# Kernel tuning notes

Hardware: AMD Instinct MI355X
Metric: run time of the kernel (lower is better)

## Reference

```python
import jax, jax.numpy as jnp
import numpy as np

EMB = 1024
HEADS = 16
HEAD_DIM = EMB // HEADS
EPS = 1e-5


def gelu_tanh(x):
    c = jnp.sqrt(jnp.asarray(2.0 / jnp.pi, x.dtype))
    return 0.5 * x * (1.0 + jnp.tanh(c * (x + 0.044715 * x ** 3)))


def layernorm(x, scale, shift):
    mean = jnp.mean(x, axis=-1, keepdims=True)
    var = jnp.mean((x - mean) ** 2, axis=-1, keepdims=True)
    return scale * (x - mean) / jnp.sqrt(var + EPS) + shift


def setup_inputs() -> dict:
    key = jax.random.key(0)
    ks = jax.random.split(key, 12)
    s = 0.02
    return {
        "x": jax.random.normal(ks[0], (2, 2048, EMB), dtype=jnp.float32),
        "Wq": jax.random.normal(ks[1], (EMB, EMB), dtype=jnp.float32) * s,
        "Wk": jax.random.normal(ks[2], (EMB, EMB), dtype=jnp.float32) * s,
        "Wv": jax.random.normal(ks[3], (EMB, EMB), dtype=jnp.float32) * s,
        "Wo": jax.random.normal(ks[4], (EMB, EMB), dtype=jnp.float32) * s,
        "bo": jnp.zeros((EMB,), dtype=jnp.float32),
        "W1": jax.random.normal(ks[5], (EMB, 4 * EMB), dtype=jnp.float32) * s,
        "b1": jnp.zeros((4 * EMB,), dtype=jnp.float32),
        "W2": jax.random.normal(ks[6], (4 * EMB, EMB), dtype=jnp.float32) * s,
        "b2": jnp.zeros((EMB,), dtype=jnp.float32),
        "ln1_scale": jnp.ones((EMB,), dtype=jnp.float32),
        "ln1_shift": jnp.zeros((EMB,), dtype=jnp.float32),
        "ln2_scale": jnp.ones((EMB,), dtype=jnp.float32),
        "ln2_shift": jnp.zeros((EMB,), dtype=jnp.float32),
    }


def reference(x, Wq, Wk, Wv, Wo, bo, W1, b1, W2, b2,
              ln1_scale, ln1_shift, ln2_scale, ln2_shift):
    b, n, d = x.shape
    # --- attention sublayer (pre-LN) ---
    h = layernorm(x, ln1_scale, ln1_shift)
    q = (h @ Wq).reshape(b, n, HEADS, HEAD_DIM).transpose(0, 2, 1, 3)  # [b,h,n,hd]
    k = (h @ Wk).reshape(b, n, HEADS, HEAD_DIM).transpose(0, 2, 1, 3)
    v = (h @ Wv).reshape(b, n, HEADS, HEAD_DIM).transpose(0, 2, 1, 3)
    scores = jnp.einsum('bhqd,bhkd->bhqk', q, k)  # [b,h,n,n]
    causal = jnp.tril(jnp.ones((n, n), dtype=bool))  # True = keep
    scores = jnp.where(causal, scores, -jnp.inf)
    weights = jax.nn.softmax(scores / np.sqrt(HEAD_DIM), axis=-1)
    ctx = jnp.einsum('bhqk,bhkd->bqhd', weights, v).reshape(b, n, d)
    attn_out = ctx @ Wo + bo
    x = x + attn_out
    # --- FFN sublayer (pre-LN) ---
    h = layernorm(x, ln2_scale, ln2_shift)
    h = gelu_tanh(h @ W1 + b1) @ W2 + b2
    return x + h
```

## Files before the change

### kernel.cpp

```cpp
#include <hip/hip_runtime.h>
#include <hip/hip_bf16.h>


using bf16 = __hip_bfloat16;
using bf16x8 = __attribute__((ext_vector_type(8))) short;
using f32x4 = __attribute__((ext_vector_type(4))) float;

#define MFMA16(a, b, c) __builtin_amdgcn_mfma_f32_16x16x32_bf16((a), (b), (c), 0, 0, 0)

enum { EPI_BF16 = 0, EPI_BIAS_RES_F32 = 1, EPI_GELU_BF16 = 2 };

__device__ __forceinline__ float cvt_f(float x) { return x; }
__device__ __forceinline__ float cvt_f(bf16 x) { return __bfloat162float(x); }

__device__ __forceinline__ float gelu_f(float x) {
  float z = 0.7978845608028654f * (x + 0.044715f * x * x * x);
  z = fminf(fmaxf(z, -15.f), 15.f);
  float e = __expf(2.f * z);
  return 0.5f * x * (1.f + (e - 1.f) / (e + 1.f));
}

__device__ __forceinline__ void stage16(const bf16* g, bf16* lds_base, int lane) {
#if defined(__has_builtin) && __has_builtin(__builtin_amdgcn_global_load_lds)
  __builtin_amdgcn_global_load_lds(
      (__attribute__((address_space(1))) void*)(void*)g,
      (__attribute__((address_space(3))) void*)lds_base, 16, 0, 0);
#else
  *(int4*)(lds_base + lane * 8) = *(const int4*)g;
#endif
}

template <typename T>
__global__ __launch_bounds__(256) void transpose_bf16_k(
    const T* __restrict__ src, bf16* __restrict__ dst, int sld, int dld) {
  __shared__ float tile[32][33];
  const int tx = threadIdx.x & 31, ty = threadIdx.x >> 5;
  const size_t r0 = (size_t)blockIdx.y * 32, c0 = (size_t)blockIdx.x * 32;
#pragma unroll
  for (int i = 0; i < 32; i += 8)
    tile[ty + i][tx] = cvt_f(src[(r0 + ty + i) * sld + c0 + tx]);
  __syncthreads();
#pragma unroll
  for (int i = 0; i < 32; i += 8)
    dst[(c0 + ty + i) * dld + r0 + tx] = __float2bfloat16(tile[tx][ty + i]);
}

__global__ __launch_bounds__(256) void ln_fwd_k(
    const float* __restrict__ x, const float* __restrict__ gam,
    const float* __restrict__ bet, bf16* __restrict__ out) {
  const int row = blockIdx.x;
  const float4 v = ((const float4*)(x + (size_t)row * 1024))[threadIdx.x];
  float s = v.x + v.y + v.z + v.w;
  float sq = v.x * v.x + v.y * v.y + v.z * v.z + v.w * v.w;
#pragma unroll
  for (int off = 32; off; off >>= 1) {
    s += __shfl_down(s, off);
    sq += __shfl_down(sq, off);
  }
  __shared__ float rs[4], rq[4];
  const int w = threadIdx.x >> 6, lane = threadIdx.x & 63;
  if (lane == 0) { rs[w] = s; rq[w] = sq; }
  __syncthreads();
  s = rs[0] + rs[1] + rs[2] + rs[3];
  sq = rq[0] + rq[1] + rq[2] + rq[3];
  const float mean = s * (1.f / 1024.f);
  const float var = sq * (1.f / 1024.f) - mean * mean;
  const float rstd = rsqrtf(var + 1e-5f);
  const float4 g4 = ((const float4*)gam)[threadIdx.x];
  const float4 b4 = ((const float4*)bet)[threadIdx.x];
  short4 pk;
  bf16* hp = (bf16*)&pk;
  hp[0] = __float2bfloat16((v.x - mean) * rstd * g4.x + b4.x);
  hp[1] = __float2bfloat16((v.y - mean) * rstd * g4.y + b4.y);
  hp[2] = __float2bfloat16((v.z - mean) * rstd * g4.z + b4.z);
  hp[3] = __float2bfloat16((v.w - mean) * rstd * g4.w + b4.w);
  ((short4*)(out + (size_t)row * 1024))[threadIdx.x] = pk;
}

template <int EPI, int BN>
__global__ __launch_bounds__(256) void gemm_bt_k(
    const bf16* __restrict__ A, const bf16* __restrict__ BT,
    void* __restrict__ Cout, const float* __restrict__ bias,
    const float* __restrict__ res, int M, int N, int K) {
  constexpr int WC = BN / 64;
  constexpr int MI = 2 * WC;
  __shared__ bf16 As[128 * 64];
  __shared__ bf16 Bs[BN * 64];
  const int tid = threadIdx.x;
  const int w = tid >> 6, lane = tid & 63;
  const int wc = w % WC, wr = w / WC;
  const int lr = lane & 15, lk = lane >> 4;
  const size_t rowTile = (size_t)blockIdx.y * 128;
  const size_t colTile = (size_t)blockIdx.x * BN;

  const bf16* Ag = A + rowTile * K;
  const bf16* Bg = BT + colTile * K;
  const int srow = lane >> 3;
  const int scol = (lane & 7) * 8;

  const f32x4 z4 = {0.f, 0.f, 0.f, 0.f};
  f32x4 acc[MI][4];
#pragma unroll
  for (int i = 0; i < MI; ++i)
#pragma unroll
    for (int j = 0; j < 4; ++j) acc[i][j] = z4;

  for (int kb = 0; kb < K; kb += 64) {
#pragma unroll
    for (int i = 0; i < 4; ++i) {
      const int r = w * 32 + i * 8;
      stage16(Ag + (size_t)(r + srow) * K + kb + scol, &As[r * 64], lane);
    }
#pragma unroll
    for (int i = 0; i < BN / 32; ++i) {
      const int r = w * (BN / 4) + i * 8;
      stage16(Bg + (size_t)(r + srow) * K + kb + scol, &Bs[r * 64], lane);
    }
    __syncthreads();
#pragma unroll
    for (int kk = 0; kk < 2; ++kk) {
      bf16x8 af[MI], bg[4];
#pragma unroll
      for (int mi = 0; mi < MI; ++mi)
        af[mi] = *(const bf16x8*)&As[(wr * (32 * WC) + mi * 16 + lr) * 64 + kk * 32 + lk * 8];
#pragma unroll
      for (int ni = 0; ni < 4; ++ni)
        bg[ni] = *(const bf16x8*)&Bs[(wc * 64 + ni * 16 + lr) * 64 + kk * 32 + lk * 8];
#pragma unroll
      for (int mi = 0; mi < MI; ++mi)
#pragma unroll
        for (int ni = 0; ni < 4; ++ni)
          acc[mi][ni] = MFMA16(af[mi], bg[ni], acc[mi][ni]);
    }
    __syncthreads();
  }

  const size_t baseRow = rowTile + wr * (32 * WC);
  const size_t baseCol = colTile + wc * 64;
#pragma unroll
  for (int mi = 0; mi < MI; ++mi)
#pragma unroll
    for (int ni = 0; ni < 4; ++ni) {
      const size_t col = baseCol + ni * 16 + lr;
#pragma unroll
      for (int r = 0; r < 4; ++r) {
        const size_t row = baseRow + mi * 16 + lk * 4 + r;
        const size_t idx = row * (size_t)N + col;
        const float v = acc[mi][ni][r];
        if constexpr (EPI == EPI_BF16) {
          ((bf16*)Cout)[idx] = __float2bfloat16(v);
        } else if constexpr (EPI == EPI_BIAS_RES_F32) {
          ((float*)Cout)[idx] = v + bias[col] + res[idx];
        } else {
          ((bf16*)Cout)[idx] = __float2bfloat16(gelu_f(v + bias[col]));
        }
      }
    }
}

__global__ __launch_bounds__(256) void attn_fwd_k(
    const bf16* __restrict__ QKV, const bf16* __restrict__ VT,
    bf16* __restrict__ ctx) {
  const int qp = blockIdx.x, head = blockIdx.y, batch = blockIdx.z;
  const int tid = threadIdx.x;
  const int w = tid >> 6, lane = tid & 63;
  const int lr = lane & 15, lk = lane >> 4;
  const int qbA = qp, qbB = 31 - qp;
  const int qrowA = qbA * 64 + w * 16;
  const int qrowB = qbB * 64 + w * 16;

  __shared__ bf16 Ks[64 * 64];
  __shared__ bf16 Vs[64 * 64];
  __shared__ bf16 Ps[4][16 * 64];

  const bf16* qpa = QKV + (size_t)(batch * 2048 + qrowA + lr) * 3072 + head * 64 + lk * 8;
  const bf16* qpb = QKV + (size_t)(batch * 2048 + qrowB + lr) * 3072 + head * 64 + lk * 8;
  const bf16x8 aqA0 = *(const bf16x8*)qpa, aqA1 = *(const bf16x8*)(qpa + 32);
  const bf16x8 aqB0 = *(const bf16x8*)qpb, aqB1 = *(const bf16x8*)(qpb + 32);

  const f32x4 z4 = {0.f, 0.f, 0.f, 0.f};
  float mA[4], lA[4], mB[4], lB[4];
  f32x4 coA[4], coB[4];
#pragma unroll
  for (int r = 0; r < 4; ++r) { mA[r] = mB[r] = -1e30f; lA[r] = lB[r] = 0.f; }
#pragma unroll
  for (int nd = 0; nd < 4; ++nd) { coA[nd] = z4; coB[nd] = z4; }

  const bf16* kbase = QKV + (size_t)(batch * 2048) * 3072 + 1024 + head * 64;
  const bf16* vbase = VT + (size_t)(head * 64) * 4096 + batch * 2048;
  const int srow = tid >> 3;
  const int scol = (tid & 7) * 8;
  const int swoff = ((tid & 7) ^ (srow & 7)) * 8;
  const int eQ = (lk ^ (lr & 7)) << 3;

  auto attn_step = [&](int qrow_w, bool diag, int kb64, float* m0, float* l0,
                       f32x4* co, bf16x8 aq0, bf16x8 aq1) {
    f32x4 sv[4];
#pragma unroll
    for (int ni = 0; ni < 4; ++ni) {
      const bf16x8 bk0 = *(const bf16x8*)&Ks[(ni * 16 + lr) * 64 + eQ];
      const bf16x8 bk1 = *(const bf16x8*)&Ks[(ni * 16 + lr) * 64 + (eQ ^ 32)];
      f32x4 z = z4;
      z = MFMA16(aq0, bk0, z);
      z = MFMA16(aq1, bk1, z);
      sv[ni] = z;
    }
#pragma unroll
    for (int ni = 0; ni < 4; ++ni)
#pragma unroll
      for (int r = 0; r < 4; ++r) {
        float v = sv[ni][r] * 0.125f;
        if (diag && (kb64 + ni * 16 + lr > qrow_w + lk * 4 + r)) v = -1e30f;
        sv[ni][r] = v;
      }
    float fac[4];
#pragma unroll
    for (int r = 0; r < 4; ++r) {
      float mx = fmaxf(fmaxf(sv[0][r], sv[1][r]), fmaxf(sv[2][r], sv[3][r]));
      mx = fmaxf(mx, __shfl_xor(mx, 1));
      mx = fmaxf(mx, __shfl_xor(mx, 2));
      mx = fmaxf(mx, __shfl_xor(mx, 4));
      mx = fmaxf(mx, __shfl_xor(mx, 8));
      const float mn = fmaxf(m0[r], mx);
      fac[r] = __expf(m0[r] - mn);
      m0[r] = mn;
    }
#pragma unroll
    for (int ni = 0; ni < 4; ++ni)
#pragma unroll
      for (int r = 0; r < 4; ++r) sv[ni][r] = __expf(sv[ni][r] - m0[r]);
#pragma unroll
    for (int r = 0; r < 4; ++r) {
      float ps = sv[0][r] + sv[1][r] + sv[2][r] + sv[3][r];
      ps += __shfl_xor(ps, 1);
      ps += __shfl_xor(ps, 2);
      ps += __shfl_xor(ps, 4);
      ps += __shfl_xor(ps, 8);
      l0[r] = l0[r] * fac[r] + ps;
    }
#pragma unroll
    for (int ni = 0; ni < 4; ++ni)
#pragma unroll
      for (int r = 0; r < 4; ++r) {
        const int prow = lk * 4 + r;
        const int pcol = (((ni * 2 + (lr >> 3)) ^ (prow & 7)) << 3) + (lr & 7);
        Ps[w][prow * 64 + pcol] = __float2bfloat16(sv[ni][r]);
      }
#pragma unroll
    for (int nd = 0; nd < 4; ++nd)
#pragma unroll
      for (int r = 0; r < 4; ++r) co[nd][r] *= fac[r];
#pragma unroll
    for (int kk = 0; kk < 2; ++kk) {
      const int ep = kk ? (eQ ^ 32) : eQ;
      const bf16x8 ap = *(const bf16x8*)&Ps[w][lr * 64 + ep];
#pragma unroll
      for (int nd = 0; nd < 4; ++nd) {
        const bf16x8 bv = *(const bf16x8*)&Vs[(nd * 16 + lr) * 64 + ep];
        co[nd] = MFMA16(ap, bv, co[nd]);
      }
    }
  };

  for (int kb = 0; kb <= qbB; ++kb) {
    const int kb64 = kb * 64;
    *(int4*)&Ks[srow * 64 + swoff]        = *(const int4*)&kbase[(size_t)(kb64 + srow) * 3072 + scol];
    *(int4*)&Ks[(srow + 32) * 64 + swoff] = *(const int4*)&kbase[(size_t)(kb64 + srow + 32) * 3072 + scol];
    *(int4*)&Vs[srow * 64 + swoff]        = *(const int4*)&vbase[(size_t)srow * 4096 + kb64 + scol];
    *(int4*)&Vs[(srow + 32) * 64 + swoff] = *(const int4*)&vbase[(size_t)(srow + 32) * 4096 + kb64 + scol];
    __syncthreads();

    attn_step(qrowB, kb == qbB, kb64, mB, lB, coB, aqB0, aqB1);
    if (kb <= qbA)
      attn_step(qrowA, kb == qbA, kb64, mA, lA, coA, aqA0, aqA1);
    __syncthreads();
  }

#pragma unroll
  for (int nd = 0; nd < 4; ++nd)
#pragma unroll
    for (int r = 0; r < 4; ++r) {
      const size_t rowA = (size_t)(batch * 2048 + qrowA + lk * 4 + r);
      ctx[rowA * 1024 + head * 64 + nd * 16 + lr] = __float2bfloat16(coA[nd][r] / lA[r]);
      const size_t rowB = (size_t)(batch * 2048 + qrowB + lk * 4 + r);
      ctx[rowB * 1024 + head * 64 + nd * 16 + lr] = __float2bfloat16(coB[nd][r] / lB[r]);
    }
}

extern "C" void kernel_launch(void* const* d_in, const int* in_sizes, int n_in,
                              void* d_out, int out_size, void* d_ws, size_t ws_size,
                              hipStream_t stream) {
  const float* x    = (const float*)d_in[0];
  const float* Wq   = (const float*)d_in[1];
  const float* Wk   = (const float*)d_in[2];
  const float* Wv   = (const float*)d_in[3];
  const float* Wo   = (const float*)d_in[4];
  const float* bo   = (const float*)d_in[5];
  const float* W1   = (const float*)d_in[6];
  const float* b1   = (const float*)d_in[7];
  const float* W2   = (const float*)d_in[8];
  const float* b2   = (const float*)d_in[9];
  const float* ln1s = (const float*)d_in[10];
  const float* ln1b = (const float*)d_in[11];
  const float* ln2s = (const float*)d_in[12];
  const float* ln2b = (const float*)d_in[13];
  float* out = (float*)d_out;

  char* ws = (char*)d_ws;
  const size_t MB = 1ull << 20;
  bf16* WqkvT = (bf16*)(ws + 0);
  bf16* WoT   = (bf16*)(ws + 6 * MB);
  bf16* W1T   = (bf16*)(ws + 8 * MB);
  bf16* W2T   = (bf16*)(ws + 16 * MB);
  bf16* h1    = (bf16*)(ws + 24 * MB);
  bf16* QKV   = (bf16*)(ws + 32 * MB);
  bf16* VT    = (bf16*)(ws + 56 * MB);
  bf16* f1    = (bf16*)(ws + 32 * MB);
  bf16* ctx   = (bf16*)(ws + 64 * MB);

  const dim3 T(256);

  transpose_bf16_k<float><<<dim3(32, 32), T, 0, stream>>>(Wq, WqkvT, 1024, 1024);
  transpose_bf16_k<float><<<dim3(32, 32), T, 0, stream>>>(Wk, WqkvT + 1024 * 1024, 1024, 1024);
  transpose_bf16_k<float><<<dim3(32, 32), T, 0, stream>>>(Wv, WqkvT + 2048 * 1024, 1024, 1024);
  transpose_bf16_k<float><<<dim3(32, 32), T, 0, stream>>>(Wo, WoT, 1024, 1024);
  transpose_bf16_k<float><<<dim3(128, 32), T, 0, stream>>>(W1, W1T, 4096, 1024);
  transpose_bf16_k<float><<<dim3(32, 128), T, 0, stream>>>(W2, W2T, 1024, 4096);

  ln_fwd_k<<<4096, T, 0, stream>>>(x, ln1s, ln1b, h1);

  gemm_bt_k<EPI_BF16, 128><<<dim3(24, 32), T, 0, stream>>>(
      h1, WqkvT, QKV, nullptr, nullptr, 4096, 3072, 1024);

  transpose_bf16_k<bf16><<<dim3(32, 128), T, 0, stream>>>(QKV + 2048, VT, 3072, 4096);

  attn_fwd_k<<<dim3(16, 16, 2), T, 0, stream>>>(QKV, VT, ctx);

  gemm_bt_k<EPI_BIAS_RES_F32, 64><<<dim3(16, 32), T, 0, stream>>>(
      ctx, WoT, out, bo, x, 4096, 1024, 1024);

  ln_fwd_k<<<4096, T, 0, stream>>>(out, ln2s, ln2b, h1);

  gemm_bt_k<EPI_GELU_BF16, 128><<<dim3(32, 32), T, 0, stream>>>(
      h1, W1T, f1, b1, nullptr, 4096, 4096, 1024);

  gemm_bt_k<EPI_BIAS_RES_F32, 64><<<dim3(16, 32), T, 0, stream>>>(
      f1, W2T, out, b2, out, 4096, 1024, 4096);
}
```

Before: 424.3 us.

## Split paired-query attention blocks into one query block per workgroup, use exp2

```diff
diff --git a/kernel.cpp b/kernel.cpp
--- a/kernel.cpp
+++ b/kernel.cpp
@@ -12,6 +12,14 @@
 
 __device__ __forceinline__ float cvt_f(float x) { return x; }
 __device__ __forceinline__ float cvt_f(bf16 x) { return __bfloat162float(x); }
+
+__device__ __forceinline__ float fast_exp2(float x) {
+#if defined(__has_builtin) && __has_builtin(__builtin_amdgcn_exp2f)
+  return __builtin_amdgcn_exp2f(x);
+#else
+  return exp2f(x);
+#endif
+}
 
 __device__ __forceinline__ float gelu_f(float x) {
   float z = 0.7978845608028654f * (x + 0.044715f * x * x * x);
@@ -161,30 +169,28 @@
 __global__ __launch_bounds__(256) void attn_fwd_k(
     const bf16* __restrict__ QKV, const bf16* __restrict__ VT,
     bf16* __restrict__ ctx) {
-  const int qp = blockIdx.x, head = blockIdx.y, batch = blockIdx.z;
+  const int qb = 31 - blockIdx.x;
+  const int head = blockIdx.y, batch = blockIdx.z;
   const int tid = threadIdx.x;
   const int w = tid >> 6, lane = tid & 63;
   const int lr = lane & 15, lk = lane >> 4;
-  const int qbA = qp, qbB = 31 - qp;
-  const int qrowA = qbA * 64 + w * 16;
-  const int qrowB = qbB * 64 + w * 16;
+  const int qrow_w = qb * 64 + w * 16;
 
   __shared__ bf16 Ks[64 * 64];
   __shared__ bf16 Vs[64 * 64];
   __shared__ bf16 Ps[4][16 * 64];
 
-  const bf16* qpa = QKV + (size_t)(batch * 2048 + qrowA + lr) * 3072 + head * 64 + lk * 8;
-  const bf16* qpb = QKV + (size_t)(batch * 2048 + qrowB + lr) * 3072 + head * 64 + lk * 8;
-  const bf16x8 aqA0 = *(const bf16x8*)qpa, aqA1 = *(const bf16x8*)(qpa + 32);
-  const bf16x8 aqB0 = *(const bf16x8*)qpb, aqB1 = *(const bf16x8*)(qpb + 32);
+  const bf16* qp = QKV + (size_t)(batch * 2048 + qrow_w + lr) * 3072 + head * 64 + lk * 8;
+  const bf16x8 aq0 = *(const bf16x8*)qp;
+  const bf16x8 aq1 = *(const bf16x8*)(qp + 32);
 
   const f32x4 z4 = {0.f, 0.f, 0.f, 0.f};
-  float mA[4], lA[4], mB[4], lB[4];
-  f32x4 coA[4], coB[4];
-#pragma unroll
-  for (int r = 0; r < 4; ++r) { mA[r] = mB[r] = -1e30f; lA[r] = lB[r] = 0.f; }
-#pragma unroll
-  for (int nd = 0; nd < 4; ++nd) { coA[nd] = z4; coB[nd] = z4; }
+  float m0[4], l0[4];
+  f32x4 co[4];
+#pragma unroll
+  for (int r = 0; r < 4; ++r) { m0[r] = -1e30f; l0[r] = 0.f; }
+#pragma unroll
+  for (int nd = 0; nd < 4; ++nd) co[nd] = z4;
 
   const bf16* kbase = QKV + (size_t)(batch * 2048) * 3072 + 1024 + head * 64;
   const bf16* vbase = VT + (size_t)(head * 64) * 4096 + batch * 2048;
@@ -193,8 +199,16 @@
   const int swoff = ((tid & 7) ^ (srow & 7)) * 8;
   const int eQ = (lk ^ (lr & 7)) << 3;
 
-  auto attn_step = [&](int qrow_w, bool diag, int kb64, float* m0, float* l0,
-                       f32x4* co, bf16x8 aq0, bf16x8 aq1) {
+  const float SCALE = 0.125f * 1.44269504f;
+
+  for (int kb = 0; kb <= qb; ++kb) {
+    const int kb64 = kb * 64;
+    *(int4*)&Ks[srow * 64 + swoff]        = *(const int4*)&kbase[(size_t)(kb64 + srow) * 3072 + scol];
+    *(int4*)&Ks[(srow + 32) * 64 + swoff] = *(const int4*)&kbase[(size_t)(kb64 + srow + 32) * 3072 + scol];
+    *(int4*)&Vs[srow * 64 + swoff]        = *(const int4*)&vbase[(size_t)srow * 4096 + kb64 + scol];
+    *(int4*)&Vs[(srow + 32) * 64 + swoff] = *(const int4*)&vbase[(size_t)(srow + 32) * 4096 + kb64 + scol];
+    __syncthreads();
+
     f32x4 sv[4];
 #pragma unroll
     for (int ni = 0; ni < 4; ++ni) {
@@ -205,11 +219,12 @@
       z = MFMA16(aq1, bk1, z);
       sv[ni] = z;
     }
+    const bool diag = (kb == qb);
 #pragma unroll
     for (int ni = 0; ni < 4; ++ni)
 #pragma unroll
       for (int r = 0; r < 4; ++r) {
-        float v = sv[ni][r] * 0.125f;
+        float v = sv[ni][r] * SCALE;
         if (diag && (kb64 + ni * 16 + lr > qrow_w + lk * 4 + r)) v = -1e30f;
         sv[ni][r] = v;
       }
@@ -222,13 +237,13 @@
       mx = fmaxf(mx, __shfl_xor(mx, 4));
       mx = fmaxf(mx, __shfl_xor(mx, 8));
       const float mn = fmaxf(m0[r], mx);
-      fac[r] = __expf(m0[r] - mn);
+      fac[r] = fast_exp2(m0[r] - mn);
       m0[r] = mn;
     }
 #pragma unroll
     for (int ni = 0; ni < 4; ++ni)
 #pragma unroll
-      for (int r = 0; r < 4; ++r) sv[ni][r] = __expf(sv[ni][r] - m0[r]);
+      for (int r = 0; r < 4; ++r) sv[ni][r] = fast_exp2(sv[ni][r] - m0[r]);
 #pragma unroll
     for (int r = 0; r < 4; ++r) {
       float ps = sv[0][r] + sv[1][r] + sv[2][r] + sv[3][r];
@@ -260,19 +275,6 @@
         co[nd] = MFMA16(ap, bv, co[nd]);
       }
     }
-  };
-
-  for (int kb = 0; kb <= qbB; ++kb) {
-    const int kb64 = kb * 64;
-    *(int4*)&Ks[srow * 64 + swoff]        = *(const int4*)&kbase[(size_t)(kb64 + srow) * 3072 + scol];
-    *(int4*)&Ks[(srow + 32) * 64 + swoff] = *(const int4*)&kbase[(size_t)(kb64 + srow + 32) * 3072 + scol];
-    *(int4*)&Vs[srow * 64 + swoff]        = *(const int4*)&vbase[(size_t)srow * 4096 + kb64 + scol];
-    *(int4*)&Vs[(srow + 32) * 64 + swoff] = *(const int4*)&vbase[(size_t)(srow + 32) * 4096 + kb64 + scol];
-    __syncthreads();
-
-    attn_step(qrowB, kb == qbB, kb64, mB, lB, coB, aqB0, aqB1);
-    if (kb <= qbA)
-      attn_step(qrowA, kb == qbA, kb64, mA, lA, coA, aqA0, aqA1);
     __syncthreads();
   }
 
@@ -280,10 +282,9 @@
   for (int nd = 0; nd < 4; ++nd)
 #pragma unroll
     for (int r = 0; r < 4; ++r) {
-      const size_t rowA = (size_t)(batch * 2048 + qrowA + lk * 4 + r);
-      ctx[rowA * 1024 + head * 64 + nd * 16 + lr] = __float2bfloat16(coA[nd][r] / lA[r]);
-      const size_t rowB = (size_t)(batch * 2048 + qrowB + lk * 4 + r);
-      ctx[rowB * 1024 + head * 64 + nd * 16 + lr] = __float2bfloat16(coB[nd][r] / lB[r]);
+      const float v = co[nd][r] / l0[r];
+      const size_t row = (size_t)(batch * 2048 + qrow_w + lk * 4 + r);
+      ctx[row * 1024 + head * 64 + nd * 16 + lr] = __float2bfloat16(v);
     }
 }
 
@@ -334,7 +335,7 @@
 
   transpose_bf16_k<bf16><<<dim3(32, 128), T, 0, stream>>>(QKV + 2048, VT, 3072, 4096);
 
-  attn_fwd_k<<<dim3(16, 16, 2), T, 0, stream>>>(QKV, VT, ctx);
+  attn_fwd_k<<<dim3(32, 16, 2), T, 0, stream>>>(QKV, VT, ctx);
 
   gemm_bt_k<EPI_BIAS_RES_F32, 64><<<dim3(16, 32), T, 0, stream>>>(
       ctx, WoT, out, bo, x, 4096, 1024, 1024);
```

Result: slower. 475.1 us (+12.0%).
